# Optimization experiments

Measured on AMD Instinct MI355X. Metric: run time of the kernel, lower is better.

Reference implementation:

```python
import jax, jax.numpy as jnp
import numpy as np

B, O, I, F, KS, H, W = 32, 64, 64, 16, 3, 128, 128


def setup_inputs() -> dict:
    key = jax.random.key(0)
    k1, k2, k3, k4 = jax.random.split(key, 4)
    addresses = jax.random.normal(k1, (B, O, I + 1, F), dtype=jnp.float32)
    x = jax.random.normal(k2, (B, I, H, W), dtype=jnp.float32)
    # kaiming-uniform-ish init for the (F, ks, ks) filter bank
    fan_in = KS * KS
    bound_w = np.sqrt(6.0 / ((1 + 5.0) * fan_in))  # kaiming_uniform a=sqrt(5)
    w_bank = jax.random.uniform(k3, (F, KS, KS), minval=-bound_w, maxval=bound_w, dtype=jnp.float32)
    bound_b = 1.0 / np.sqrt(fan_in)
    b_bank = jax.random.uniform(k4, (F,), minval=-bound_b, maxval=bound_b, dtype=jnp.float32)
    return {"addresses": addresses, "x": x, "w_bank": w_bank, "b_bank": b_bank, "s": 1, "p": 1}


def reference(addresses, x, w_bank, b_bank, s, p):
    # addresses: (B, O, I+1, F); slice off the bias address on dim 2
    w_addr = addresses[:, :, 1:]   # (B, O, I, F)
    b_addr = addresses[:, :, 0]    # (B, O, F)
    # soft routing over the filter bank (softmax over num_filters)
    aw = jax.nn.softmax(w_addr, axis=-1)
    w = jnp.einsum('boif,fkl->boikl', aw, w_bank)  # per-sample conv weights (B, O, I, ks, ks)
    ab = jax.nn.softmax(b_addr, axis=-1)
    b = jnp.einsum('bof,f->bo', ab, b_bank)        # per-sample bias (B, O)

    def conv_one(xi, wi):
        # xi: (I, H, W), wi: (O, I, ks, ks)
        y = jax.lax.conv_general_dilated(
            xi[None], wi, window_strides=(s, s),
            padding=[(p, p), (p, p)],
            dimension_numbers=('NCHW', 'OIHW', 'NCHW'))
        return y[0]  # (O, H', W')

    y = jax.vmap(conv_one)(x, w)  # per-example dynamic conv (groups=batch)
    return y + b[:, :, None, None]
```

## Files before the change

kernel.cpp:

```cpp
#include <hip/hip_runtime.h>

#define BB 32
#define OO 64
#define II 64
#define FF 16
#define HH 128
#define WW 128

typedef __attribute__((ext_vector_type(8))) __bf16 bf16x8;
typedef __attribute__((ext_vector_type(4))) float f32x4;

typedef __attribute__((address_space(3))) uint8_t  lds_u8;
typedef __attribute__((address_space(1))) const uint8_t g_u8;

__global__ __launch_bounds__(64)
void gen_weights(const float* __restrict__ addr,
                 const float* __restrict__ w_bank,
                 const float* __restrict__ b_bank,
                 __bf16* __restrict__ wT,
                 float* __restrict__ bias_out) {
    const int bo  = blockIdx.x;
    const int tid = threadIdx.x;

    __shared__ float bank_s[FF * 9];
    __shared__ float bbank_s[FF];
    for (int idx = tid; idx < FF * 9; idx += 64) bank_s[idx] = w_bank[idx];
    if (tid < FF) bbank_s[tid] = b_bank[tid];
    __syncthreads();

    const float* arow = addr + ((size_t)bo * (II + 1) + 1 + tid) * FF;
    float a[FF];
    float m = -1e30f;
#pragma unroll
    for (int f = 0; f < FF; ++f) { a[f] = arow[f]; m = fmaxf(m, a[f]); }
    float s = 0.f;
#pragma unroll
    for (int f = 0; f < FF; ++f) { a[f] = __expf(a[f] - m); s += a[f]; }
    const float inv = 1.0f / s;

    const int b = bo >> 6, o = bo & 63;
#pragma unroll
    for (int kl = 0; kl < 9; ++kl) {
        float acc = 0.f;
#pragma unroll
        for (int f = 0; f < FF; ++f) acc += a[f] * bank_s[f * 9 + kl];
        wT[(((size_t)b * 9 + kl) * OO + o) * II + tid] = (__bf16)(acc * inv);
    }

    if (tid == 0) {
        const float* brow = addr + (size_t)bo * (II + 1) * FF;
        float bb[FF];
        float bm = -1e30f;
#pragma unroll
        for (int f = 0; f < FF; ++f) { bb[f] = brow[f]; bm = fmaxf(bm, bb[f]); }
        float bs = 0.f;
#pragma unroll
        for (int f = 0; f < FF; ++f) { bb[f] = __expf(bb[f] - bm); bs += bb[f]; }
        float acc = 0.f;
#pragma unroll
        for (int f = 0; f < FF; ++f) acc += bb[f] * bbank_s[f];
        bias_out[bo] = acc / bs;
    }
}

#define SLOTB 8448
#define NSLOT 10
#define RINGOFF 73728
#define LDSZ (RINGOFF + NSLOT * SLOTB)

#define LOADPAIR(pr_) do {                                                         \
    const int pxg_ = ph * 64 + l - 1;                                              \
    const bool okpx_ = (unsigned)pxg_ < 128u;                                      \
    _Pragma("unroll")                                                              \
    for (int j_ = 0; j_ < 2; ++j_) {                                               \
        const int gr_ = R0 + (pr_) + j_ - 1;                                       \
        const bool ok_ = okpx_ && ((unsigned)gr_ < 128u);                          \
        const float* xs_ = xb + ((size_t)(wv * 8) * HH + gr_) * WW + pxg_;         \
        float* dst_ = j_ ? sm1 : sm0;                                              \
        _Pragma("unroll")                                                          \
        for (int jj_ = 0; jj_ < 8; ++jj_) {                                        \
            float v_ = 0.f;                                                        \
            if (ok_) v_ = xs_[(size_t)jj_ * (HH * WW)];                            \
            dst_[jj_] = v_;                                                        \
        }                                                                          \
    }                                                                              \
    {               \
        const int lr_ = l >> 4;                                                    \
        const int cc_ = (l >> 1) & 7;                                              \
        const int pxl_ = 64 + (l & 1);                                             \
        const int pxg2_ = ph * 64 + pxl_ - 1;                                      \
        const int gr_ = R0 + (pr_) + lr_ - 1;                                      \
        const bool ok_ = (t < 32) && ((unsigned)pxg2_ < 128u)                      \
                         && ((unsigned)gr_ < 128u);                                \
        const float* xs_ = xb + ((size_t)(cc_ * 8) * HH + gr_) * WW + pxg2_;       \
        _Pragma("unroll")                                                          \
        for (int jj_ = 0; jj_ < 8; ++jj_) {                                        \
            float v_ = 0.f;                                                        \
            if (ok_) v_ = xs_[(size_t)jj_ * (HH * WW)];                            \
            smt[jj_] = v_;                                                         \
        }                                                                          \
    }                                                                              \
} while (0)

#define WRITEPAIR(sA_, sB_) do {                                                   \
    bf16x8 u_;                                                                     \
    _Pragma("unroll")                                                              \
    for (int jj_ = 0; jj_ < 8; ++jj_) u_[jj_] = (__bf16)sm0[jj_];                  \
    *(bf16x8*)(LDS + RINGOFF + (sA_) * SLOTB + l * 128                             \
               + ((wv ^ (l & 7)) << 4)) = u_;                                      \
    _Pragma("unroll")                                                              \
    for (int jj_ = 0; jj_ < 8; ++jj_) u_[jj_] = (__bf16)sm1[jj_];                  \
    *(bf16x8*)(LDS + RINGOFF + (sB_) * SLOTB + l * 128                             \
               + ((wv ^ (l & 7)) << 4)) = u_;                                      \
    if (t < 32) {                                                                  \
        const int lr_ = l >> 4;                                                    \
        const int cc_ = (l >> 1) & 7;                                              \
        const int pxl_ = 64 + (l & 1);                                             \
        const int sl_ = lr_ ? (sB_) : (sA_);                                       \
        _Pragma("unroll")                                                          \
        for (int jj_ = 0; jj_ < 8; ++jj_) u_[jj_] = (__bf16)smt[jj_];              \
        *(bf16x8*)(LDS + RINGOFF + sl_ * SLOTB + pxl_ * 128                        \
                   + ((cc_ ^ (pxl_ & 7)) << 4)) = u_;                              \
    }                                                                              \
} while (0)

#define KS_RANGE(K0_, K1_) do {                                                    \
    _Pragma("unroll")                                                              \
    for (int ks = (K0_); ks < (K1_); ++ks) {                                       \
        const int kl = ks >> 1, k0 = ks & 1;                                       \
        const int dr = kl / 3, dc = kl - 3 * dr;                                   \
        const int cc = lk + 4 * k0;                                                \
        bf16x8 af[2], bv[4];                                                       \
        _Pragma("unroll")                                                          \
        for (int mf = 0; mf < 2; ++mf)                                             \
            af[mf] = *(const bf16x8*)(LDS + kl * 8192 + (obase0 + mf * 16) * 128   \
                                      + ((cc ^ (lm & 7)) << 4));                   \
        const int lpx = pxbase + dc;                                               \
        const int swb = lpx * 128 + ((cc ^ (lpx & 7)) << 4);                       \
        _Pragma("unroll")                                                          \
        for (int nf = 0; nf < 4; ++nf)                                             \
            bv[nf] = *(const bf16x8*)(LDS + off_[nf + dr] + swb);                  \
        _Pragma("unroll")                                                          \
        for (int mf = 0; mf < 2; ++mf)                                             \
            _Pragma("unroll")                                                      \
            for (int nf = 0; nf < 4; ++nf)                                         \
                acc[mf][nf] = __builtin_amdgcn_mfma_f32_16x16x32_bf16(             \
                    af[mf], bv[nf], acc[mf][nf], 0, 0, 0);                         \
    }                                                                              \
} while (0)

__global__ __launch_bounds__(512, 2)
void conv_fused(const float* __restrict__ x, const __bf16* __restrict__ wT,
                const float* __restrict__ bias, float* __restrict__ y) {
    __shared__ __align__(16) char LDS[LDSZ];

    const int hwid = blockIdx.x;
    const int work = (hwid & 7) * 32 + (hwid >> 3);
    const int b  = work >> 3;
    const int r3 = work & 7;
    const int ph = r3 >> 2;
    const int rg = r3 & 3;
    const int R0 = rg * 32;

    const int t  = threadIdx.x;
    const int wv = t >> 6;
    const int l  = t & 63;
    const int lm = l & 15;
    const int lk = l >> 4;
    const int oh = wv >> 2;
    const int g  = wv & 3;

    const __bf16* wb = wT + (size_t)b * 9 * OO * II;
    const float*  xb = x + (size_t)b * II * HH * WW;

#pragma unroll
    for (int it = 0; it < 9; ++it) {
        const int cid = it * 512 + t;
        const int kl  = cid >> 9;
        const int rem = cid & 511;
        const int o   = rem >> 3;
        const int c   = rem & 7;
        const __bf16* src = wb + ((kl * 64 + o) << 6) + ((c ^ (o & 7)) << 3);
        __builtin_amdgcn_global_load_lds((g_u8*)src,
            (lds_u8*)(LDS + (size_t)(it * 512 + (t & 448)) * 16), 16, 0, 0);
    }

    float sm0[8], sm1[8], smt[8];

    LOADPAIR(0); WRITEPAIR(0, 1);
    LOADPAIR(2); WRITEPAIR(2, 3);
    LOADPAIR(4); WRITEPAIR(4, 5);

    float bbias[2][4];
    {
        const float* bp = bias + b * OO;
#pragma unroll
        for (int mf = 0; mf < 2; ++mf)
#pragma unroll
            for (int r = 0; r < 4; ++r)
                bbias[mf][r] = bp[oh * 32 + mf * 16 + lk * 4 + r];
    }
    f32x4 acc[2][4];
#pragma unroll
    for (int mf = 0; mf < 2; ++mf)
#pragma unroll
        for (int nf = 0; nf < 4; ++nf)
#pragma unroll
            for (int r = 0; r < 4; ++r)
                acc[mf][nf][r] = bbias[mf][r];

    __syncthreads();

    const int pxbase = g * 16 + lm;
    const int obase0 = oh * 32 + lm;

    int s0 = 0;
    for (int p = 0; p < 8; ++p) {
        int off_[6];
#pragma unroll
        for (int d = 0; d < 6; ++d) {
            int ss = s0 + d; if (ss >= NSLOT) ss -= NSLOT;
            off_[d] = RINGOFF + ss * SLOTB;
        }
        int wA = s0 + 6; if (wA >= NSLOT) wA -= NSLOT;
        int wB = wA + 1; if (wB >= NSLOT) wB -= NSLOT;
        int wC = wB + 1; if (wC >= NSLOT) wC -= NSLOT;
        int wD = wC + 1; if (wD >= NSLOT) wD -= NSLOT;
        const int pr = 4 * p;
        const bool pf = (p < 7);

        if (pf) LOADPAIR(pr + 6);
        KS_RANGE(0, 9);
        if (pf) { WRITEPAIR(wA, wB); LOADPAIR(pr + 8); }
        KS_RANGE(9, 18);
        if (pf) WRITEPAIR(wC, wD);

        __syncthreads();

#pragma unroll
        for (int mf = 0; mf < 2; ++mf)
#pragma unroll
            for (int r = 0; r < 4; ++r) {
                const int o = oh * 32 + mf * 16 + lk * 4 + r;
#pragma unroll
                for (int nf = 0; nf < 4; ++nf) {
                    const int rowg = R0 + pr + nf;
                    y[(((size_t)b * OO + o) * HH + rowg) * WW + ph * 64 + pxbase]
                        = acc[mf][nf][r];
                }
            }
#pragma unroll
        for (int mf = 0; mf < 2; ++mf)
#pragma unroll
            for (int nf = 0; nf < 4; ++nf)
#pragma unroll
                for (int r = 0; r < 4; ++r)
                    acc[mf][nf][r] = bbias[mf][r];

        s0 += 4; if (s0 >= NSLOT) s0 -= NSLOT;
    }
}

extern "C" void kernel_launch(void* const* d_in, const int* in_sizes, int n_in,
                              void* d_out, int out_size, void* d_ws, size_t ws_size,
                              hipStream_t stream) {
    const float* addresses = (const float*)d_in[0];
    const float* x         = (const float*)d_in[1];
    const float* w_bank    = (const float*)d_in[2];
    const float* b_bank    = (const float*)d_in[3];
    float* out = (float*)d_out;

    float*  bias_ws = (float*)d_ws;
    __bf16* wT      = (__bf16*)((char*)d_ws + 8192);

    gen_weights<<<BB * OO, 64, 0, stream>>>(addresses, w_bank, b_bank, wT, bias_ws);
    conv_fused<<<256, 512, 0, stream>>>(x, wT, bias_ws, out);
}
```

Before: 96.31 us.

## Switch conv MFMA tiling to 32x32x16 with per-wave row/column split

```diff
diff --git a/kernel.cpp b/kernel.cpp
--- a/kernel.cpp
+++ b/kernel.cpp
@@ -9,6 +9,7 @@
 
 typedef __attribute__((ext_vector_type(8))) __bf16 bf16x8;
 typedef __attribute__((ext_vector_type(4))) float f32x4;
+typedef __attribute__((ext_vector_type(16))) float f32x16;
 
 typedef __attribute__((address_space(3))) uint8_t  lds_u8;
 typedef __attribute__((address_space(1))) const uint8_t g_u8;
@@ -65,10 +66,11 @@
 
 #define SLOTB 8448
 #define NSLOT 10
-#define RINGOFF 73728
-#define LDSZ (RINGOFF + NSLOT * SLOTB)
-
-#define LOADPAIR(pr_) do {                                                         \
+#define RING  73728
+#define BIASOFF (RING + NSLOT * SLOTB)
+#define LDSZ (BIASOFF + 256)
+
+#define LOADPAIR(pr_, s0_, s1_, st_) do {                                          \
     const int pxg_ = ph * 64 + l - 1;                                              \
     const bool okpx_ = (unsigned)pxg_ < 128u;                                      \
     _Pragma("unroll")                                                              \
@@ -76,7 +78,7 @@
         const int gr_ = R0 + (pr_) + j_ - 1;                                       \
         const bool ok_ = okpx_ && ((unsigned)gr_ < 128u);                          \
         const float* xs_ = xb + ((size_t)(wv * 8) * HH + gr_) * WW + pxg_;         \
-        float* dst_ = j_ ? sm1 : sm0;                                              \
+        float* dst_ = j_ ? (s1_) : (s0_);                                          \
         _Pragma("unroll")                                                          \
         for (int jj_ = 0; jj_ < 8; ++jj_) {                                        \
             float v_ = 0.f;                                                        \
@@ -97,20 +99,20 @@
         for (int jj_ = 0; jj_ < 8; ++jj_) {                                        \
             float v_ = 0.f;                                                        \
             if (ok_) v_ = xs_[(size_t)jj_ * (HH * WW)];                            \
-            smt[jj_] = v_;                                                         \
+            (st_)[jj_] = v_;                                                       \
         }                                                                          \
     }                                                                              \
 } while (0)
 
-#define WRITEPAIR(sA_, sB_) do {                                                   \
+#define WRITEPAIR(sA_, sB_, s0_, s1_, st_) do {                                    \
     bf16x8 u_;                                                                     \
     _Pragma("unroll")                                                              \
-    for (int jj_ = 0; jj_ < 8; ++jj_) u_[jj_] = (__bf16)sm0[jj_];                  \
-    *(bf16x8*)(LDS + RINGOFF + (sA_) * SLOTB + l * 128                             \
+    for (int jj_ = 0; jj_ < 8; ++jj_) u_[jj_] = (__bf16)(s0_)[jj_];                \
+    *(bf16x8*)(LDS + RING + (sA_) * SLOTB + l * 128                                \
                + ((wv ^ (l & 7)) << 4)) = u_;                                      \
     _Pragma("unroll")                                                              \
-    for (int jj_ = 0; jj_ < 8; ++jj_) u_[jj_] = (__bf16)sm1[jj_];                  \
-    *(bf16x8*)(LDS + RINGOFF + (sB_) * SLOTB + l * 128                             \
+    for (int jj_ = 0; jj_ < 8; ++jj_) u_[jj_] = (__bf16)(s1_)[jj_];                \
+    *(bf16x8*)(LDS + RING + (sB_) * SLOTB + l * 128                                \
                + ((wv ^ (l & 7)) << 4)) = u_;                                      \
     if (t < 32) {                                                                  \
         const int lr_ = l >> 4;                                                    \
@@ -118,8 +120,8 @@
         const int pxl_ = 64 + (l & 1);                                             \
         const int sl_ = lr_ ? (sB_) : (sA_);                                       \
         _Pragma("unroll")                                                          \
-        for (int jj_ = 0; jj_ < 8; ++jj_) u_[jj_] = (__bf16)smt[jj_];              \
-        *(bf16x8*)(LDS + RINGOFF + sl_ * SLOTB + pxl_ * 128                        \
+        for (int jj_ = 0; jj_ < 8; ++jj_) u_[jj_] = (__bf16)(st_)[jj_];            \
+        *(bf16x8*)(LDS + RING + sl_ * SLOTB + pxl_ * 128                           \
                    + ((cc_ ^ (pxl_ & 7)) << 4)) = u_;                              \
     }                                                                              \
 } while (0)
@@ -127,29 +129,22 @@
 #define KS_RANGE(K0_, K1_) do {                                                    \
     _Pragma("unroll")                                                              \
     for (int ks = (K0_); ks < (K1_); ++ks) {                                       \
-        const int kl = ks >> 1, k0 = ks & 1;                                       \
+        const int kl = ks >> 2, s = ks & 3;                                        \
         const int dr = kl / 3, dc = kl - 3 * dr;                                   \
-        const int cc = lk + 4 * k0;                                                \
-        bf16x8 af[2], bv[4];                                                       \
-        _Pragma("unroll")                                                          \
-        for (int mf = 0; mf < 2; ++mf)                                             \
-            af[mf] = *(const bf16x8*)(LDS + kl * 8192 + (obase0 + mf * 16) * 128   \
-                                      + ((cc ^ (lm & 7)) << 4));                   \
-        const int lpx = pxbase + dc;                                               \
-        const int swb = lpx * 128 + ((cc ^ (lpx & 7)) << 4);                       \
-        _Pragma("unroll")                                                          \
-        for (int nf = 0; nf < 4; ++nf)                                             \
-            bv[nf] = *(const bf16x8*)(LDS + off_[nf + dr] + swb);                  \
-        _Pragma("unroll")                                                          \
-        for (int mf = 0; mf < 2; ++mf)                                             \
-            _Pragma("unroll")                                                      \
-            for (int nf = 0; nf < 4; ++nf)                                         \
-                acc[mf][nf] = __builtin_amdgcn_mfma_f32_16x16x32_bf16(             \
-                    af[mf], bv[nf], acc[mf][nf], 0, 0, 0);                         \
+        const int ck = 2 * s + lhi;                      \
+        const bf16x8 af0 = *(const bf16x8*)(LDS + kl * 8192 + l31 * 128            \
+                              + ((ck ^ l7) << 4));                                 \
+        const bf16x8 af1 = *(const bf16x8*)(LDS + kl * 8192 + (32 + l31) * 128     \
+                              + ((ck ^ l7) << 4));                                 \
+        const int pxl = q * 32 + l31 + dc;                                         \
+        const bf16x8 bv = *(const bf16x8*)(LDS + o3[dr] + pxl * 128                \
+                              + ((ck ^ (pxl & 7)) << 4));                          \
+        acc0 = __builtin_amdgcn_mfma_f32_32x32x16_bf16(af0, bv, acc0, 0, 0, 0);    \
+        acc1 = __builtin_amdgcn_mfma_f32_32x32x16_bf16(af1, bv, acc1, 0, 0, 0);    \
     }                                                                              \
 } while (0)
 
-__global__ __launch_bounds__(512, 2)
+__global__ __launch_bounds__(512, 1)
 void conv_fused(const float* __restrict__ x, const __bf16* __restrict__ wT,
                 const float* __restrict__ bias, float* __restrict__ y) {
     __shared__ __align__(16) char LDS[LDSZ];
@@ -165,10 +160,9 @@
     const int t  = threadIdx.x;
     const int wv = t >> 6;
     const int l  = t & 63;
-    const int lm = l & 15;
-    const int lk = l >> 4;
-    const int oh = wv >> 2;
-    const int g  = wv & 3;
+    const int r  = wv >> 1;
+    const int q  = wv & 1;
+    const int l31 = l & 31, lhi = l >> 5, l7 = l & 7;
 
     const __bf16* wb = wT + (size_t)b * 9 * OO * II;
     const float*  xb = x + (size_t)b * II * HH * WW;
@@ -184,44 +178,25 @@
         __builtin_amdgcn_global_load_lds((g_u8*)src,
             (lds_u8*)(LDS + (size_t)(it * 512 + (t & 448)) * 16), 16, 0, 0);
     }
-
-    float sm0[8], sm1[8], smt[8];
-
-    LOADPAIR(0); WRITEPAIR(0, 1);
-    LOADPAIR(2); WRITEPAIR(2, 3);
-    LOADPAIR(4); WRITEPAIR(4, 5);
-
-    float bbias[2][4];
-    {
-        const float* bp = bias + b * OO;
-#pragma unroll
-        for (int mf = 0; mf < 2; ++mf)
-#pragma unroll
-            for (int r = 0; r < 4; ++r)
-                bbias[mf][r] = bp[oh * 32 + mf * 16 + lk * 4 + r];
-    }
-    f32x4 acc[2][4];
-#pragma unroll
-    for (int mf = 0; mf < 2; ++mf)
-#pragma unroll
-        for (int nf = 0; nf < 4; ++nf)
-#pragma unroll
-            for (int r = 0; r < 4; ++r)
-                acc[mf][nf][r] = bbias[mf][r];
+    if (t < 64) *(float*)(LDS + BIASOFF + t * 4) = bias[b * OO + t];
+
+    float smA0[8], smA1[8], smAt[8];
+
+    LOADPAIR(0, smA0, smA1, smAt); WRITEPAIR(0, 1, smA0, smA1, smAt);
+    LOADPAIR(2, smA0, smA1, smAt); WRITEPAIR(2, 3, smA0, smA1, smAt);
+    LOADPAIR(4, smA0, smA1, smAt); WRITEPAIR(4, 5, smA0, smA1, smAt);
+
+    f32x16 acc0 = {}, acc1 = {};
 
     __syncthreads();
-
-    const int pxbase = g * 16 + lm;
-    const int obase0 = oh * 32 + lm;
 
     int s0 = 0;
     for (int p = 0; p < 8; ++p) {
-        int off_[6];
-#pragma unroll
-        for (int d = 0; d < 6; ++d) {
-            int ss = s0 + d; if (ss >= NSLOT) ss -= NSLOT;
-            off_[d] = RINGOFF + ss * SLOTB;
-        }
+        int d0_ = s0 + r;  if (d0_ >= NSLOT) d0_ -= NSLOT;
+        int d1_ = d0_ + 1; if (d1_ >= NSLOT) d1_ -= NSLOT;
+        int d2_ = d1_ + 1; if (d2_ >= NSLOT) d2_ -= NSLOT;
+        const int o3[3] = { RING + d0_ * SLOTB, RING + d1_ * SLOTB,
+                            RING + d2_ * SLOTB };
         int wA = s0 + 6; if (wA >= NSLOT) wA -= NSLOT;
         int wB = wA + 1; if (wB >= NSLOT) wB -= NSLOT;
         int wC = wB + 1; if (wC >= NSLOT) wC -= NSLOT;
@@ -229,33 +204,38 @@
         const int pr = 4 * p;
         const bool pf = (p < 7);
 
-        if (pf) LOADPAIR(pr + 6);
-        KS_RANGE(0, 9);
-        if (pf) { WRITEPAIR(wA, wB); LOADPAIR(pr + 8); }
-        KS_RANGE(9, 18);
-        if (pf) WRITEPAIR(wC, wD);
+        float smB0[8], smB1[8], smBt[8];
+
+        if (pf) LOADPAIR(pr + 6, smA0, smA1, smAt);
+        KS_RANGE(0, 18);
+        if (pf) {
+            LOADPAIR(pr + 8, smB0, smB1, smBt);
+            WRITEPAIR(wA, wB, smA0, smA1, smAt);
+        }
+        KS_RANGE(18, 36);
+        if (pf) WRITEPAIR(wC, wD, smB0, smB1, smBt);
 
         __syncthreads();
 
-#pragma unroll
-        for (int mf = 0; mf < 2; ++mf)
-#pragma unroll
-            for (int r = 0; r < 4; ++r) {
-                const int o = oh * 32 + mf * 16 + lk * 4 + r;
-#pragma unroll
-                for (int nf = 0; nf < 4; ++nf) {
-                    const int rowg = R0 + pr + nf;
-                    y[(((size_t)b * OO + o) * HH + rowg) * WW + ph * 64 + pxbase]
-                        = acc[mf][nf][r];
+        const int row = R0 + pr + r;
+        const int col = ph * 64 + q * 32 + l31;
+#pragma unroll
+        for (int mo = 0; mo < 2; ++mo) {
+#pragma unroll
+            for (int g = 0; g < 4; ++g) {
+                const f32x4 bb = *(const f32x4*)(LDS + BIASOFF
+                                   + (mo * 32 + 8 * g + 4 * lhi) * 4);
+#pragma unroll
+                for (int j = 0; j < 4; ++j) {
+                    const int o = mo * 32 + 8 * g + 4 * lhi + j;
+                    const float v = (mo ? acc1[4 * g + j] : acc0[4 * g + j])
+                                    + bb[j];
+                    y[(((size_t)b * OO + o) * HH + row) * WW + col] = v;
                 }
             }
-#pragma unroll
-        for (int mf = 0; mf < 2; ++mf)
-#pragma unroll
-            for (int nf = 0; nf < 4; ++nf)
-#pragma unroll
-                for (int r = 0; r < 4; ++r)
-                    acc[mf][nf][r] = bbias[mf][r];
+        }
+        acc0 = f32x16{};
+        acc1 = f32x16{};
 
         s0 += 4; if (s0 >= NSLOT) s0 -= NSLOT;
     }
```

Measured after the change: 134.2 us. 1.39x slower.
